# Kernel tuning notes

Hardware: AMD Instinct MI355X
Metric: run time of the kernel (lower is better)

Reference implementation:

```python
import jax, jax.numpy as jnp
import numpy as np

N_AGENTS = 512
HID = 256
OBS = 128


def setup_inputs() -> dict:
    key = jax.random.key(0)
    ks = jax.random.split(key, 10)
    s = 0.02  # weight init scale
    f32 = jnp.float32
    return {
        "inputs": jax.random.normal(ks[0], (N_AGENTS, OBS), f32),
        "fc1_w": jax.random.normal(ks[1], (HID, OBS), f32) * s,
        "fc1_b": jnp.zeros((HID,), f32),
        "in_proj_w": jax.random.normal(ks[2], (3 * HID, HID), f32) * s,
        "in_proj_b": jnp.zeros((3 * HID,), f32),
        "out_proj_w": jax.random.normal(ks[3], (HID, HID), f32) * s,
        "out_proj_b": jnp.zeros((HID,), f32),
        "fc2_w": jax.random.normal(ks[4], (HID, 2 * HID), f32) * s,
        "fc2_b": jnp.zeros((HID,), f32),
        "fc3_w": jax.random.normal(ks[5], (2, HID), f32) * s,
        "fc3_b": jnp.zeros((2,), f32),
        "vfc2_w": jax.random.normal(ks[6], (HID, HID * N_AGENTS), f32) * s,
        "vfc2_b": jnp.zeros((HID,), f32),
        "vfc3_w": jax.random.normal(ks[7], (1, HID), f32) * s,
        "vfc3_b": jnp.zeros((1,), f32),
    }


def reference(inputs, fc1_w, fc1_b, in_proj_w, in_proj_b, out_proj_w, out_proj_b,
              fc2_w, fc2_b, fc3_w, fc3_b, vfc2_w, vfc2_b, vfc3_w, vfc3_b):
    n = inputs.shape[0]
    d = fc1_w.shape[0]
    # per-agent embed
    hid = jax.nn.relu(inputs @ fc1_w.T + fc1_b)                 # [n, d]
    # single-head self-attention (torch MultiheadAttention, 1 head)
    qkv = hid @ in_proj_w.T + in_proj_b                         # [n, 3d]
    q, k, v = jnp.split(qkv, 3, axis=-1)
    scores = (q @ k.T) / jnp.sqrt(jnp.asarray(d, hid.dtype))    # [n, n]
    attn = jax.nn.softmax(scores, axis=-1)
    h = (attn @ v) @ out_proj_w.T + out_proj_b                  # [n, d]
    # all-pairs edge features restricted to strict upper triangle
    iu0, iu1 = jnp.triu_indices(n, 1)                           # P = n(n-1)/2
    pairs = jnp.concatenate([h[iu0], h[iu1]], axis=1)           # [P, 2d]
    x = jax.nn.relu(pairs @ fc2_w.T + fc2_b)                    # [P, d]
    action_out = jax.nn.softmax(x @ fc3_w.T + fc3_b, axis=-1)   # [P, 2]
    # value head over flattened node embeddings
    vh = jax.nn.relu(hid.reshape(1, -1) @ vfc2_w.T + vfc2_b)    # [1, d]
    value = vh @ vfc3_w.T + vfc3_b                              # [1, 1]
    value = jnp.broadcast_to(value, (action_out.shape[0], 1))   # [P, 1]
    return jnp.concatenate([action_out, value], axis=1)         # [P, 3]
```

## Files before the change

kernel.cpp:

```cpp
#include <hip/hip_runtime.h>
#include <math.h>

#define N_AG   512
#define HIDD   256
#define OBSD   128

__device__ __forceinline__ void fma4(float4& acc, float4 a, float4 b){
    acc.x += a.x*b.x; acc.y += a.y*b.y; acc.z += a.z*b.z; acc.w += a.w*b.w;
}
__device__ __forceinline__ float hsum(float4 a){ return (a.x+a.y)+(a.z+a.w); }

__device__ __forceinline__ void stage_rows(float* dst, const float* __restrict__ src,
        int row0, int stride, int colbase, int t){
    #pragma unroll
    for (int half = 0; half < 2; ++half){
        int idx = half*256 + t;
        int row = idx >> 3, c4 = idx & 7;
        float4 v = *(const float4*)(src + (row0+row)*stride + colbase + c4*4);
        dst[(c4*4+0)*68 + row] = v.x;
        dst[(c4*4+1)*68 + row] = v.y;
        dst[(c4*4+2)*68 + row] = v.z;
        dst[(c4*4+3)*68 + row] = v.w;
    }
}
__device__ __forceinline__ void tile_compute(const float* As, const float* Bs,
        int tx, int ty, float4 acc[4]){
    #pragma unroll
    for (int kk = 0; kk < 32; ++kk){
        float4 a = *(const float4*)(As + kk*68 + ty*4);
        float4 b = *(const float4*)(Bs + kk*68 + tx*4);
        acc[0].x += a.x*b.x; acc[0].y += a.x*b.y; acc[0].z += a.x*b.z; acc[0].w += a.x*b.w;
        acc[1].x += a.y*b.x; acc[1].y += a.y*b.y; acc[1].z += a.y*b.z; acc[1].w += a.y*b.w;
        acc[2].x += a.z*b.x; acc[2].y += a.z*b.y; acc[2].z += a.z*b.z; acc[2].w += a.z*b.w;
        acc[3].x += a.w*b.x; acc[3].y += a.w*b.y; acc[3].z += a.w*b.z; acc[3].w += a.w*b.w;
    }
}

__global__ __launch_bounds__(256, 2) void k_fc1(const float* __restrict__ in,
        const float* __restrict__ w, const float* __restrict__ b,
        float* __restrict__ hid){
    __shared__ float lin[8*OBSD];
    int at = blockIdx.y, ot = blockIdx.x, t = threadIdx.x;
    ((float4*)lin)[t] = ((const float4*)(in + at*8*OBSD))[t];
    __syncthreads();
    int ol = t & 63, g = t >> 6;
    int o = ot*64 + ol;
    const float4* w4 = (const float4*)(w + o*OBSD);
    const float4* la = (const float4*)(lin + (g*2)*OBSD);
    const float4* lb = (const float4*)(lin + (g*2+1)*OBSD);
    float4 a0 = {0,0,0,0}, a1 = {0,0,0,0};
    #pragma unroll
    for (int c = 0; c < OBSD/4; ++c){
        float4 wv = w4[c];
        fma4(a0, la[c], wv);
        fma4(a1, lb[c], wv);
    }
    float bb = b[o];
    int ag = at*8 + g*2;
    hid[ag*HIDD + o]     = fmaxf(hsum(a0) + bb, 0.f);
    hid[(ag+1)*HIDD + o] = fmaxf(hsum(a1) + bb, 0.f);
}

__global__ __launch_bounds__(256, 2) void k_qkv(const float* __restrict__ hid,
        const float* __restrict__ w, const float* __restrict__ b,
        float* __restrict__ qkv){
    __shared__ float lin[8*HIDD];
    int at = blockIdx.y, ot = blockIdx.x, t = threadIdx.x;
    const float4* in4 = (const float4*)(hid + at*8*HIDD);
    ((float4*)lin)[t]       = in4[t];
    ((float4*)lin)[t + 256] = in4[t + 256];
    __syncthreads();
    int ol = t & 63, g = t >> 6;
    int o = ot*64 + ol;
    const float4* w4 = (const float4*)(w + o*HIDD);
    const float4* la = (const float4*)(lin + (g*2)*HIDD);
    const float4* lb = (const float4*)(lin + (g*2+1)*HIDD);
    float4 a0 = {0,0,0,0}, a1 = {0,0,0,0};
    #pragma unroll 8
    for (int c = 0; c < HIDD/4; ++c){
        float4 wv = w4[c];
        fma4(a0, la[c], wv);
        fma4(a1, lb[c], wv);
    }
    float bb = b[o];
    int ag = at*8 + g*2;
    qkv[ag*768 + o]     = hsum(a0) + bb;
    qkv[(ag+1)*768 + o] = hsum(a1) + bb;
}

__global__ __launch_bounds__(256, 2) void k_big(const float* __restrict__ qkv,
        const float* __restrict__ ow, const float* __restrict__ hid,
        const float* __restrict__ vw_w, float* __restrict__ S,
        float* __restrict__ VW, float* __restrict__ partial){
    __shared__ float As[32*68];
    __shared__ float Bs[32*68];
    int t = threadIdx.x;
    int bid = blockIdx.x;
    if (bid < 64){
        int ti = bid >> 3, tj = bid & 7;
        int i0 = ti*64, j0 = tj*64;
        int tx = t & 15, ty = t >> 4;
        float4 acc[4] = {{0,0,0,0},{0,0,0,0},{0,0,0,0},{0,0,0,0}};
        for (int k0 = 0; k0 < 256; k0 += 32){
            __syncthreads();
            stage_rows(As, qkv, i0, 768, k0,       t);
            stage_rows(Bs, qkv, j0, 768, 256 + k0, t);
            __syncthreads();
            tile_compute(As, Bs, tx, ty, acc);
        }
        #pragma unroll
        for (int r = 0; r < 4; ++r){
            float4 o;
            o.x = acc[r].x*0.0625f; o.y = acc[r].y*0.0625f;
            o.z = acc[r].z*0.0625f; o.w = acc[r].w*0.0625f;
            *(float4*)(S + (i0+ty*4+r)*512 + j0 + tx*4) = o;
        }
        return;
    }
    if (bid < 96){
        int b2 = bid - 64;
        int ti = b2 >> 2, tj = b2 & 3;
        int j0 = ti*64, d0 = tj*64;
        int tx = t & 15, ty = t >> 4;
        float4 acc[4] = {{0,0,0,0},{0,0,0,0},{0,0,0,0},{0,0,0,0}};
        for (int k0 = 0; k0 < 256; k0 += 32){
            __syncthreads();
            stage_rows(As, qkv, j0, 768, 512 + k0, t);
            stage_rows(Bs, ow,  d0, 256, k0,       t);
            __syncthreads();
            tile_compute(As, Bs, tx, ty, acc);
        }
        #pragma unroll
        for (int r = 0; r < 4; ++r)
            *(float4*)(VW + (j0+ty*4+r)*256 + d0 + tx*4) = acc[r];
        return;
    }
    int id = bid - 96;
    int chunk = id & 7, o = id >> 3;
    const float4* h4 = (const float4*)hid;
    const float4* w4 = (const float4*)vw_w;
    long base  = (long)chunk*4096;
    long wbase = (long)o*32768 + base;
    float4 aa = {0,0,0,0}, ab = {0,0,0,0};
    #pragma unroll 4
    for (int it = 0; it < 8; ++it){
        fma4(aa, h4[base + it*256 + t],     w4[wbase + it*256 + t]);
        fma4(ab, h4[base + (it+8)*256 + t], w4[wbase + (it+8)*256 + t]);
    }
    float acc = hsum(aa) + hsum(ab);
    for (int off = 32; off; off >>= 1) acc += __shfl_xor(acc, off);
    int lane = t & 63, wid = t >> 6;
    if (lane == 0) As[wid] = acc;
    __syncthreads();
    if (t == 0) partial[o*8 + chunk] = As[0]+As[1]+As[2]+As[3];
}

__global__ __launch_bounds__(256, 2) void k_softmax(float* __restrict__ S){
    int t = threadIdx.x, w = t >> 6, ln = t & 63;
    float* row = S + (blockIdx.x*4 + w)*512;
    float v[8];
    float m = -1e30f;
    #pragma unroll
    for (int k = 0; k < 8; ++k){ v[k] = row[ln + k*64]; m = fmaxf(m, v[k]); }
    for (int off = 32; off; off >>= 1) m = fmaxf(m, __shfl_xor(m, off));
    float s = 0.f;
    #pragma unroll
    for (int k = 0; k < 8; ++k){ v[k] = expf(v[k] - m); s += v[k]; }
    for (int off = 32; off; off >>= 1) s += __shfl_xor(s, off);
    float inv = 1.f / s;
    #pragma unroll
    for (int k = 0; k < 8; ++k) row[ln + k*64] = v[k]*inv;
}

__global__ __launch_bounds__(256, 2) void k_h(const float* __restrict__ P,
        const float* __restrict__ VW, const float* __restrict__ ob,
        float* __restrict__ hout){
    __shared__ float As[32*68];
    __shared__ float Bs[32*68];
    int bid = blockIdx.x;
    int ti = bid >> 2, tj = bid & 3;
    int i0 = ti*64, d0 = tj*64;
    int t = threadIdx.x, tx = t & 15, ty = t >> 4;
    float4 acc[4] = {{0,0,0,0},{0,0,0,0},{0,0,0,0},{0,0,0,0}};
    for (int k0 = 0; k0 < 512; k0 += 32){
        __syncthreads();
        stage_rows(As, P, i0, 512, k0, t);
        #pragma unroll
        for (int half = 0; half < 2; ++half){
            int idx = half*256 + t;
            int kkr = idx >> 4, c4 = idx & 15;
            *(float4*)(Bs + kkr*68 + c4*4) = *(const float4*)(VW + (k0+kkr)*256 + d0 + c4*4);
        }
        __syncthreads();
        tile_compute(As, Bs, tx, ty, acc);
    }
    float4 bb = *(const float4*)(ob + d0 + tx*4);
    #pragma unroll
    for (int r = 0; r < 4; ++r){
        float4 o;
        o.x = acc[r].x + bb.x; o.y = acc[r].y + bb.y;
        o.z = acc[r].z + bb.z; o.w = acc[r].w + bb.w;
        *(float4*)(hout + (i0+ty*4+r)*256 + d0 + tx*4) = o;
    }
}

__global__ __launch_bounds__(256, 2) void k_ab_value(const float* __restrict__ hin,
        const float* __restrict__ w2, const float* __restrict__ b2,
        const float* __restrict__ partial, const float* __restrict__ vb,
        const float* __restrict__ v3w, const float* __restrict__ v3b,
        float* __restrict__ A, float* __restrict__ B, float* __restrict__ value){
    int t = threadIdx.x;
    if (blockIdx.x == 512){
        float s = vb[t];
        #pragma unroll
        for (int c = 0; c < 8; ++c) s += partial[t*8 + c];
        s = fmaxf(s, 0.f) * v3w[t];
        for (int off = 32; off; off >>= 1) s += __shfl_xor(s, off);
        __shared__ float redv[4];
        int lane = t & 63, wid = t >> 6;
        if (lane == 0) redv[wid] = s;
        __syncthreads();
        if (t == 0) value[0] = redv[0]+redv[1]+redv[2]+redv[3] + v3b[0];
        return;
    }
    __shared__ float lin[8*HIDD];
    int id = blockIdx.x, at = id >> 3, ot = id & 7;
    const float4* in4 = (const float4*)(hin + at*8*HIDD);
    ((float4*)lin)[t]       = in4[t];
    ((float4*)lin)[t + 256] = in4[t + 256];
    __syncthreads();
    int ol = t & 63, g = t >> 6;
    int o2 = ot*64 + ol;
    bool isA = o2 < HIDD;
    int o = isA ? o2 : o2 - HIDD;
    const float4* w4 = (const float4*)(w2 + o*512 + (isA ? 0 : HIDD));
    const float4* la = (const float4*)(lin + (g*2)*HIDD);
    const float4* lb = (const float4*)(lin + (g*2+1)*HIDD);
    float4 acc0 = {0,0,0,0}, acc1 = {0,0,0,0};
    #pragma unroll 8
    for (int c = 0; c < HIDD/4; ++c){
        float4 wv = w4[c];
        fma4(acc0, la[c], wv);
        fma4(acc1, lb[c], wv);
    }
    int a0 = at*8 + g*2;
    float* dst = isA ? A : B;
    float bb = isA ? b2[o] : 0.f;
    dst[a0*HIDD + o]     = hsum(acc0) + bb;
    dst[(a0+1)*HIDD + o] = hsum(acc1) + bb;
}

__global__ __launch_bounds__(256, 2) void k_pairs(const float* __restrict__ A,
        const float* __restrict__ B, const float* __restrict__ w3,
        const float* __restrict__ b3, const float* __restrict__ value,
        float* __restrict__ out){
    int ti = blockIdx.x, tj = blockIdx.y;
    if (tj < ti) return;
    __shared__ float la[16*260], lb[16*260], lw[256];
    int t = threadIdx.x;
    #pragma unroll
    for (int l = 0; l < 4; ++l){
        int idx = l*256 + t;
        int r = idx >> 6, c4 = idx & 63;
        ((float4*)la)[r*65 + c4] = ((const float4*)A)[(ti*16 + r)*64 + c4];
        ((float4*)lb)[r*65 + c4] = ((const float4*)B)[(tj*16 + r)*64 + c4];
    }
    lw[t] = w3[t] - w3[256 + t];
    __syncthreads();
    float val = value[0];
    float bd  = b3[0] - b3[1];
    int il = t >> 4, jl = t & 15;
    int i = ti*16 + il, j = tj*16 + jl;
    if (j > i){
        const float4* a4 = (const float4*)(la + il*260);
        const float4* b4 = (const float4*)(lb + jl*260);
        const float4* w4 = (const float4*)lw;
        float4 acc = {0,0,0,0};
        #pragma unroll 8
        for (int c = 0; c < 64; ++c){
            float4 aa = a4[c], bb = b4[c], wv = w4[c];
            acc.x += fmaxf(aa.x + bb.x, 0.f)*wv.x;
            acc.y += fmaxf(aa.y + bb.y, 0.f)*wv.y;
            acc.z += fmaxf(aa.z + bb.z, 0.f)*wv.z;
            acc.w += fmaxf(aa.w + bb.w, 0.f)*wv.w;
        }
        float z = hsum(acc) + bd;
        float o0 = 1.f/(1.f + expf(-z));
        int p = i*511 - (i*(i-1))/2 + (j - i - 1);
        out[3*p]   = o0;
        out[3*p+1] = 1.f - o0;
        out[3*p+2] = val;
    }
}

extern "C" void kernel_launch(void* const* d_in, const int* in_sizes, int n_in,
                              void* d_out, int out_size, void* d_ws, size_t ws_size,
                              hipStream_t stream){
    const float* inputs = (const float*)d_in[0];
    const float* fc1_w  = (const float*)d_in[1];
    const float* fc1_b  = (const float*)d_in[2];
    const float* inp_w  = (const float*)d_in[3];
    const float* inp_b  = (const float*)d_in[4];
    const float* outp_w = (const float*)d_in[5];
    const float* outp_b = (const float*)d_in[6];
    const float* fc2_w  = (const float*)d_in[7];
    const float* fc2_b  = (const float*)d_in[8];
    const float* fc3_w  = (const float*)d_in[9];
    const float* fc3_b  = (const float*)d_in[10];
    const float* vfc2_w = (const float*)d_in[11];
    const float* vfc2_b = (const float*)d_in[12];
    const float* vfc3_w = (const float*)d_in[13];
    const float* vfc3_b = (const float*)d_in[14];
    float* out = (float*)d_out;
    float* ws  = (float*)d_ws;
    float* hid     = ws;
    float* qkv     = ws + 131072;
    float* S       = ws + 524288;
    float* VW      = ws + 786432;
    float* h       = ws + 917504;
    float* A       = ws + 1048576;
    float* B       = ws + 1179648;
    float* partial = ws + 1310720;
    float* value   = ws + 1312768;

    k_fc1     <<<dim3(4, 64),  256, 0, stream>>>(inputs, fc1_w, fc1_b, hid);
    k_qkv     <<<dim3(12, 64), 256, 0, stream>>>(hid, inp_w, inp_b, qkv);
    k_big     <<<dim3(2144),   256, 0, stream>>>(qkv, outp_w, hid, vfc2_w, S, VW, partial);
    k_softmax <<<dim3(128),    256, 0, stream>>>(S);
    k_h       <<<dim3(32),     256, 0, stream>>>(S, VW, outp_b, h);
    k_ab_value<<<dim3(513),    256, 0, stream>>>(h, fc2_w, fc2_b, partial, vfc2_b, vfc3_w, vfc3_b, A, B, value);
    k_pairs   <<<dim3(32, 32), 256, 0, stream>>>(A, B, fc3_w, fc3_b, value, out);
}
```

Before: 299.3 us.

## Spread vfc2 weight streaming across all kernels with atomic row accumulation

The 128 MB vfc2 weight stream used to run only inside k_big. It is now split into 2048 units, each covering two output rows and one sixteenth of K, and these units are spread across k_qkv, k_big, k_soft, k_h and k_ab. The goal is to overlap this bandwidth-bound GEMV with the small compute-bound attention kernels. Partial sums are combined with atomicAdd into a rowacc buffer that k_fc1 zeroes. The final value reduction moves into k_pairs, which removes the separate value block, and weight reads use nontemporal loads. This adds atomic traffic, float summation order that varies between runs, and extra blocks in every launch.

Measured after the change: 309.6 us. 1.03x slower.

```diff
diff --git a/kernel.cpp b/kernel.cpp
--- a/kernel.cpp
+++ b/kernel.cpp
@@ -5,10 +5,45 @@
 #define HIDD   256
 #define OBSD   128
 
+typedef float v4f __attribute__((ext_vector_type(4)));
+
+#if __has_builtin(__builtin_nontemporal_load)
+#define NTLOAD(p) __builtin_nontemporal_load(p)
+#else
+#define NTLOAD(p) (*(p))
+#endif
+
 __device__ __forceinline__ void fma4(float4& acc, float4 a, float4 b){
     acc.x += a.x*b.x; acc.y += a.y*b.y; acc.z += a.z*b.z; acc.w += a.w*b.w;
 }
 __device__ __forceinline__ float hsum(float4 a){ return (a.x+a.y)+(a.z+a.w); }
+__device__ __forceinline__ float hsumv(v4f a){ return (a.x+a.y)+(a.z+a.w); }
+
+__device__ __forceinline__ void stream_unit(int q, int t, const float* __restrict__ hid,
+        const float* __restrict__ vw, float* __restrict__ rowacc, float* red8){
+    int rg = q >> 4, s = q & 15;
+    const v4f* h4 = (const v4f*)hid + s*2048;
+    const v4f* w0 = (const v4f*)vw + (long)(rg*2)*32768 + s*2048;
+    const v4f* w1 = w0 + 32768;
+    v4f a0 = {0,0,0,0}, a1 = {0,0,0,0};
+    #pragma unroll
+    for (int k = 0; k < 8; ++k){
+        int o = k*256 + t;
+        v4f hv = h4[o];
+        a0 += hv * NTLOAD(w0 + o);
+        a1 += hv * NTLOAD(w1 + o);
+    }
+    float s0 = hsumv(a0), s1 = hsumv(a1);
+    for (int off = 32; off; off >>= 1){
+        s0 += __shfl_xor(s0, off);
+        s1 += __shfl_xor(s1, off);
+    }
+    int lane = t & 63, wid = t >> 6;
+    if (lane == 0){ red8[wid] = s0; red8[4+wid] = s1; }
+    __syncthreads();
+    if (t == 0) atomicAdd(rowacc + rg*2,     red8[0]+red8[1]+red8[2]+red8[3]);
+    if (t == 64) atomicAdd(rowacc + rg*2 + 1, red8[4]+red8[5]+red8[6]+red8[7]);
+}
 
 __device__ __forceinline__ void stage_rows(float* dst, const float* __restrict__ src,
         int row0, int stride, int colbase, int t){
@@ -36,11 +71,12 @@
     }
 }
 
-__global__ __launch_bounds__(256, 2) void k_fc1(const float* __restrict__ in,
+__global__ __launch_bounds__(256) void k_fc1(const float* __restrict__ in,
         const float* __restrict__ w, const float* __restrict__ b,
-        float* __restrict__ hid){
+        float* __restrict__ hid, float* __restrict__ rowacc){
     __shared__ float lin[8*OBSD];
     int at = blockIdx.y, ot = blockIdx.x, t = threadIdx.x;
+    if (ot == 0 && at == 0) rowacc[t] = 0.f;
     ((float4*)lin)[t] = ((const float4*)(in + at*8*OBSD))[t];
     __syncthreads();
     int ol = t & 63, g = t >> 6;
@@ -61,11 +97,14 @@
     hid[(ag+1)*HIDD + o] = fmaxf(hsum(a1) + bb, 0.f);
 }
 
-__global__ __launch_bounds__(256, 2) void k_qkv(const float* __restrict__ hid,
+__global__ __launch_bounds__(256) void k_qkv(const float* __restrict__ hid,
         const float* __restrict__ w, const float* __restrict__ b,
+        const float* __restrict__ vw, float* __restrict__ rowacc,
         float* __restrict__ qkv){
     __shared__ float lin[8*HIDD];
-    int at = blockIdx.y, ot = blockIdx.x, t = threadIdx.x;
+    int t = threadIdx.x, bid = blockIdx.x;
+    if (bid >= 768){ stream_unit(bid - 768, t, hid, vw, rowacc, lin); return; }
+    int ot = bid % 12, at = bid / 12;
     const float4* in4 = (const float4*)(hid + at*8*HIDD);
     ((float4*)lin)[t]       = in4[t];
     ((float4*)lin)[t + 256] = in4[t + 256];
@@ -88,16 +127,17 @@
     qkv[(ag+1)*768 + o] = hsum(a1) + bb;
 }
 
-__global__ __launch_bounds__(256, 2) void k_big(const float* __restrict__ qkv,
+__global__ __launch_bounds__(256) void k_big(const float* __restrict__ qkv,
         const float* __restrict__ ow, const float* __restrict__ hid,
-        const float* __restrict__ vw_w, float* __restrict__ S,
-        float* __restrict__ VW, float* __restrict__ partial){
+        const float* __restrict__ vw, float* __restrict__ rowacc,
+        float* __restrict__ S, float* __restrict__ VW){
     __shared__ float As[32*68];
     __shared__ float Bs[32*68];
-    int t = threadIdx.x;
-    int bid = blockIdx.x;
-    if (bid < 64){
-        int ti = bid >> 3, tj = bid & 7;
+    int t = threadIdx.x, bid = blockIdx.x;
+    if (bid < 1024){ stream_unit(256 + bid, t, hid, vw, rowacc, As); return; }
+    if (bid < 1088){
+        int b2 = bid - 1024;
+        int ti = b2 >> 3, tj = b2 & 7;
         int i0 = ti*64, j0 = tj*64;
         int tx = t & 15, ty = t >> 4;
         float4 acc[4] = {{0,0,0,0},{0,0,0,0},{0,0,0,0},{0,0,0,0}};
@@ -117,47 +157,34 @@
         }
         return;
     }
-    if (bid < 96){
-        int b2 = bid - 64;
-        int ti = b2 >> 2, tj = b2 & 3;
-        int j0 = ti*64, d0 = tj*64;
-        int tx = t & 15, ty = t >> 4;
-        float4 acc[4] = {{0,0,0,0},{0,0,0,0},{0,0,0,0},{0,0,0,0}};
-        for (int k0 = 0; k0 < 256; k0 += 32){
-            __syncthreads();
-            stage_rows(As, qkv, j0, 768, 512 + k0, t);
-            stage_rows(Bs, ow,  d0, 256, k0,       t);
-            __syncthreads();
-            tile_compute(As, Bs, tx, ty, acc);
-        }
-        #pragma unroll
-        for (int r = 0; r < 4; ++r)
-            *(float4*)(VW + (j0+ty*4+r)*256 + d0 + tx*4) = acc[r];
+    int b2 = bid - 1088;
+    int ti = b2 >> 2, tj = b2 & 3;
+    int j0 = ti*64, d0 = tj*64;
+    int tx = t & 15, ty = t >> 4;
+    float4 acc[4] = {{0,0,0,0},{0,0,0,0},{0,0,0,0},{0,0,0,0}};
+    for (int k0 = 0; k0 < 256; k0 += 32){
+        __syncthreads();
+        stage_rows(As, qkv, j0, 768, 512 + k0, t);
+        stage_rows(Bs, ow,  d0, 256, k0,       t);
+        __syncthreads();
+        tile_compute(As, Bs, tx, ty, acc);
+    }
+    #pragma unroll
+    for (int r = 0; r < 4; ++r)
+        *(float4*)(VW + (j0+ty*4+r)*256 + d0 + tx*4) = acc[r];
+}
+
+__global__ __launch_bounds__(256) void k_soft(float* __restrict__ S,
+        const float* __restrict__ hid, const float* __restrict__ vw,
+        float* __restrict__ rowacc){
+    int t = threadIdx.x, bid = blockIdx.x;
+    if (bid < 256){
+        __shared__ float red8[8];
+        stream_unit(1280 + bid, t, hid, vw, rowacc, red8);
         return;
     }
-    int id = bid - 96;
-    int chunk = id & 7, o = id >> 3;
-    const float4* h4 = (const float4*)hid;
-    const float4* w4 = (const float4*)vw_w;
-    long base  = (long)chunk*4096;
-    long wbase = (long)o*32768 + base;
-    float4 aa = {0,0,0,0}, ab = {0,0,0,0};
-    #pragma unroll 4
-    for (int it = 0; it < 8; ++it){
-        fma4(aa, h4[base + it*256 + t],     w4[wbase + it*256 + t]);
-        fma4(ab, h4[base + (it+8)*256 + t], w4[wbase + (it+8)*256 + t]);
-    }
-    float acc = hsum(aa) + hsum(ab);
-    for (int off = 32; off; off >>= 1) acc += __shfl_xor(acc, off);
-    int lane = t & 63, wid = t >> 6;
-    if (lane == 0) As[wid] = acc;
-    __syncthreads();
-    if (t == 0) partial[o*8 + chunk] = As[0]+As[1]+As[2]+As[3];
-}
-
-__global__ __launch_bounds__(256, 2) void k_softmax(float* __restrict__ S){
-    int t = threadIdx.x, w = t >> 6, ln = t & 63;
-    float* row = S + (blockIdx.x*4 + w)*512;
+    int w = t >> 6, ln = t & 63;
+    float* row = S + ((bid-256)*4 + w)*512;
     float v[8];
     float m = -1e30f;
     #pragma unroll
@@ -172,15 +199,18 @@
     for (int k = 0; k < 8; ++k) row[ln + k*64] = v[k]*inv;
 }
 
-__global__ __launch_bounds__(256, 2) void k_h(const float* __restrict__ P,
+__global__ __launch_bounds__(256) void k_h(const float* __restrict__ P,
         const float* __restrict__ VW, const float* __restrict__ ob,
-        float* __restrict__ hout){
+        const float* __restrict__ hid, const float* __restrict__ vw,
+        float* __restrict__ rowacc, float* __restrict__ hout){
     __shared__ float As[32*68];
     __shared__ float Bs[32*68];
-    int bid = blockIdx.x;
-    int ti = bid >> 2, tj = bid & 3;
+    int t = threadIdx.x, bid = blockIdx.x;
+    if (bid < 256){ stream_unit(1536 + bid, t, hid, vw, rowacc, As); return; }
+    int b2 = bid - 256;
+    int ti = b2 >> 2, tj = b2 & 3;
     int i0 = ti*64, d0 = tj*64;
-    int t = threadIdx.x, tx = t & 15, ty = t >> 4;
+    int tx = t & 15, ty = t >> 4;
     float4 acc[4] = {{0,0,0,0},{0,0,0,0},{0,0,0,0},{0,0,0,0}};
     for (int k0 = 0; k0 < 512; k0 += 32){
         __syncthreads();
@@ -204,27 +234,14 @@
     }
 }
 
-__global__ __launch_bounds__(256, 2) void k_ab_value(const float* __restrict__ hin,
+__global__ __launch_bounds__(256) void k_ab(const float* __restrict__ hin,
         const float* __restrict__ w2, const float* __restrict__ b2,
-        const float* __restrict__ partial, const float* __restrict__ vb,
-        const float* __restrict__ v3w, const float* __restrict__ v3b,
-        float* __restrict__ A, float* __restrict__ B, float* __restrict__ value){
-    int t = threadIdx.x;
-    if (blockIdx.x == 512){
-        float s = vb[t];
-        #pragma unroll
-        for (int c = 0; c < 8; ++c) s += partial[t*8 + c];
-        s = fmaxf(s, 0.f) * v3w[t];
-        for (int off = 32; off; off >>= 1) s += __shfl_xor(s, off);
-        __shared__ float redv[4];
-        int lane = t & 63, wid = t >> 6;
-        if (lane == 0) redv[wid] = s;
-        __syncthreads();
-        if (t == 0) value[0] = redv[0]+redv[1]+redv[2]+redv[3] + v3b[0];
-        return;
-    }
+        const float* __restrict__ hid, const float* __restrict__ vw,
+        float* __restrict__ rowacc, float* __restrict__ A, float* __restrict__ B){
     __shared__ float lin[8*HIDD];
-    int id = blockIdx.x, at = id >> 3, ot = id & 7;
+    int t = threadIdx.x, bid = blockIdx.x;
+    if (bid < 256){ stream_unit(1792 + bid, t, hid, vw, rowacc, lin); return; }
+    int id = bid - 256, at = id >> 3, ot = id & 7;
     const float4* in4 = (const float4*)(hin + at*8*HIDD);
     ((float4*)lin)[t]       = in4[t];
     ((float4*)lin)[t + 256] = in4[t + 256];
@@ -250,14 +267,19 @@
     dst[(a0+1)*HIDD + o] = hsum(acc1) + bb;
 }
 
-__global__ __launch_bounds__(256, 2) void k_pairs(const float* __restrict__ A,
+__global__ __launch_bounds__(256) void k_pairs(const float* __restrict__ A,
         const float* __restrict__ B, const float* __restrict__ w3,
-        const float* __restrict__ b3, const float* __restrict__ value,
-        float* __restrict__ out){
+        const float* __restrict__ b3, const float* __restrict__ rowacc,
+        const float* __restrict__ vb, const float* __restrict__ v3w,
+        const float* __restrict__ v3b, float* __restrict__ out){
     int ti = blockIdx.x, tj = blockIdx.y;
     if (tj < ti) return;
-    __shared__ float la[16*260], lb[16*260], lw[256];
+    __shared__ float la[16*260], lb[16*260], lw[256], red4[4];
     int t = threadIdx.x;
+    float pv = fmaxf(rowacc[t] + vb[t], 0.f) * v3w[t];
+    for (int off = 32; off; off >>= 1) pv += __shfl_xor(pv, off);
+    int lane = t & 63, wid = t >> 6;
+    if (lane == 0) red4[wid] = pv;
     #pragma unroll
     for (int l = 0; l < 4; ++l){
         int idx = l*256 + t;
@@ -267,7 +289,7 @@
     }
     lw[t] = w3[t] - w3[256 + t];
     __syncthreads();
-    float val = value[0];
+    float val = red4[0]+red4[1]+red4[2]+red4[3] + v3b[0];
     float bd  = b3[0] - b3[1];
     int il = t >> 4, jl = t & 15;
     int i = ti*16 + il, j = tj*16 + jl;
@@ -320,14 +342,13 @@
     float* h       = ws + 917504;
     float* A       = ws + 1048576;
     float* B       = ws + 1179648;
-    float* partial = ws + 1310720;
-    float* value   = ws + 1312768;
-
-    k_fc1     <<<dim3(4, 64),  256, 0, stream>>>(inputs, fc1_w, fc1_b, hid);
-    k_qkv     <<<dim3(12, 64), 256, 0, stream>>>(hid, inp_w, inp_b, qkv);
-    k_big     <<<dim3(2144),   256, 0, stream>>>(qkv, outp_w, hid, vfc2_w, S, VW, partial);
-    k_softmax <<<dim3(128),    256, 0, stream>>>(S);
-    k_h       <<<dim3(32),     256, 0, stream>>>(S, VW, outp_b, h);
-    k_ab_value<<<dim3(513),    256, 0, stream>>>(h, fc2_w, fc2_b, partial, vfc2_b, vfc3_w, vfc3_b, A, B, value);
-    k_pairs   <<<dim3(32, 32), 256, 0, stream>>>(A, B, fc3_w, fc3_b, value, out);
-}
+    float* rowacc  = ws + 1310720;
+
+    k_fc1  <<<dim3(4, 64),  256, 0, stream>>>(inputs, fc1_w, fc1_b, hid, rowacc);
+    k_qkv  <<<dim3(1024),   256, 0, stream>>>(hid, inp_w, inp_b, vfc2_w, rowacc, qkv);
+    k_big  <<<dim3(1120),   256, 0, stream>>>(qkv, outp_w, hid, vfc2_w, rowacc, S, VW);
+    k_soft <<<dim3(384),    256, 0, stream>>>(S, hid, vfc2_w, rowacc);
+    k_h    <<<dim3(288),    256, 0, stream>>>(S, VW, outp_b, hid, vfc2_w, rowacc, h);
+    k_ab   <<<dim3(768),    256, 0, stream>>>(h, fc2_w, fc2_b, hid, vfc2_w, rowacc, A, B);
+    k_pairs<<<dim3(32, 32), 256, 0, stream>>>(A, B, fc3_w, fc3_b, rowacc, vfc2_b, vfc3_w, vfc3_b, out);
+}
```
